# Performance work log

Hardware: AMD Instinct MI355X
Metric: run time of the kernel (lower is better)

The kernel has to match this reference:

```python
import jax, jax.numpy as jnp
import numpy as np

B, S, HID = 4, 2048, 2048
NH, NKV = 8, 1
HD = HID // NH  # 256
G = NH // NKV   # queries per kv head
ROPE_THETA = 10000.0
NEG_INF = -1e9


def setup_inputs() -> dict:
    key = jax.random.key(0)
    ks = jax.random.split(key, 4)
    x = jax.random.normal(ks[0], (B, S, HID), jnp.float32)
    qkv_dim = (NH + 2 * NKV) * HD
    w_qkv = jax.random.normal(ks[1], (HID, qkv_dim), jnp.float32) * (HID ** -0.5)
    b_qkv = jnp.zeros((qkv_dim,), jnp.float32)
    w_o = jax.random.normal(ks[2], (NH * HD, HID), jnp.float32) * ((NH * HD) ** -0.5)
    b_o = jnp.zeros((HID,), jnp.float32)
    # rotary table: cos/sin of position*inv_freq, interleaved-pair convention
    inv_freq = 1.0 / (ROPE_THETA ** (jnp.arange(0, HD, 2, dtype=jnp.float32) / HD))
    ang = jnp.outer(jnp.arange(S, dtype=jnp.float32), inv_freq)  # [S, HD/2]
    freqs_cis = jnp.stack([jnp.cos(ang), jnp.sin(ang)], axis=-1)  # [S, HD/2, 2]
    causal = jnp.tril(jnp.ones((S, S), bool))
    mask = jnp.where(causal, 0.0, NEG_INF).astype(jnp.float32)[None, None]  # [1,1,S,S]
    return dict(x=x, w_qkv=w_qkv, b_qkv=b_qkv, w_o=w_o, b_o=b_o,
                freqs_cis=freqs_cis, mask=mask)


def _rope(t, cos, sin):
    # t: [B,S,H,D]; cos/sin: [1,S,1,D/2]; interleaved complex pairs
    tp = t.reshape(*t.shape[:-1], -1, 2)
    r, i = tp[..., 0], tp[..., 1]
    out = jnp.stack([r * cos - i * sin, r * sin + i * cos], axis=-1)
    return out.reshape(t.shape)


def reference(x, w_qkv, b_qkv, w_o, b_o, freqs_cis, mask):
    b, s, _ = x.shape
    qkv = x @ w_qkv + b_qkv
    q, k, v = jnp.split(qkv, [NH * HD, NH * HD + NKV * HD], axis=-1)
    q = q.reshape(b, s, NH, HD)
    k = k.reshape(b, s, NKV, HD)
    v = v.reshape(b, s, NKV, HD)
    cos = freqs_cis[..., 0][None, :, None, :]
    sin = freqs_cis[..., 1][None, :, None, :]
    q = _rope(q, cos, sin)
    k = _rope(k, cos, sin)
    # GQA: head h attends with kv group h // G (same layout as repeat_interleave)
    qh = q.transpose(0, 2, 1, 3).reshape(b, NKV, G, s, HD)  # [B,KV,G,S,D]
    kh = k.transpose(0, 2, 1, 3)                            # [B,KV,S,D]
    vh = v.transpose(0, 2, 1, 3)
    scores = jnp.einsum('bkgqd,bksd->bkgqs', qh, kh) * (HD ** -0.5)
    scores = scores + mask[:, :, None]  # broadcast over group dim
    attn = jax.nn.softmax(scores.astype(jnp.float32), axis=-1).astype(q.dtype)
    out = jnp.einsum('bkgqs,bksd->bkgqd', attn, vh)         # [B,KV,G,S,D]
    out = out.reshape(b, NH, s, HD).transpose(0, 2, 1, 3).reshape(b, s, NH * HD)
    return out @ w_o + b_o
```

## Files before the change

### kernel.cpp

```cpp
#include <hip/hip_runtime.h>
#include <hip/hip_bf16.h>

#define B_ 4
#define S_ 2048
#define HID_ 2048
#define NH_ 8
#define HD_ 256
#define QKVN 2560

typedef unsigned short u16;
typedef unsigned long long ull;
typedef __attribute__((ext_vector_type(4))) float f32x4;
typedef __attribute__((ext_vector_type(16))) float f32x16;
typedef __attribute__((ext_vector_type(8))) short bf16x8;

__device__ __forceinline__ float bf2f(u16 u) {
  union { unsigned int i; float f; } v; v.i = ((unsigned int)u) << 16; return v.f;
}
__device__ __forceinline__ u16 f2bf(float f) {
  union { unsigned int i; float f; } v; v.f = f;
  unsigned int r = v.i + 0x7fffu + ((v.i >> 16) & 1u);
  return (u16)(r >> 16);
}

__global__ void cast_f32_bf16(const float* __restrict__ in, u16* __restrict__ out, int n8) {
  int i = blockIdx.x * blockDim.x + threadIdx.x;
  int stride = gridDim.x * blockDim.x;
  for (; i < n8; i += stride) {
    const float4* p = (const float4*)(in + (size_t)i * 8);
    float4 a = p[0], b = p[1];
    u16 o[8] = {f2bf(a.x), f2bf(a.y), f2bf(a.z), f2bf(a.w),
                f2bf(b.x), f2bf(b.y), f2bf(b.z), f2bf(b.w)};
    *(uint4*)(out + (size_t)i * 8) = *(const uint4*)o;
  }
}

__global__ void transpose_cast(const float* __restrict__ in, u16* __restrict__ out, int R, int C) {
  __shared__ float t[32][33];
  int c0 = blockIdx.x * 32, r0 = blockIdx.y * 32;
  int tx = threadIdx.x, ty = threadIdx.y;
#pragma unroll
  for (int i = 0; i < 4; ++i)
    t[ty + i * 8][tx] = in[(size_t)(r0 + ty + i * 8) * C + c0 + tx];
  __syncthreads();
#pragma unroll
  for (int i = 0; i < 4; ++i)
    out[(size_t)(c0 + ty + i * 8) * R + r0 + tx] = f2bf(t[tx][ty + i * 8]);
}

__global__ void transpose_bf16(const u16* __restrict__ in, u16* __restrict__ out, int R, int C) {
  __shared__ u16 t[32][33];
  in += (size_t)blockIdx.z * R * C;
  out += (size_t)blockIdx.z * R * C;
  int c0 = blockIdx.x * 32, r0 = blockIdx.y * 32;
  int tx = threadIdx.x, ty = threadIdx.y;
#pragma unroll
  for (int i = 0; i < 4; ++i)
    t[ty + i * 8][tx] = in[(size_t)(r0 + ty + i * 8) * C + c0 + tx];
  __syncthreads();
#pragma unroll
  for (int i = 0; i < 4; ++i)
    out[(size_t)(c0 + ty + i * 8) * R + r0 + tx] = t[tx][ty + i * 8];
}

template <bool OUT_F32>
__global__ __launch_bounds__(256) void gemm_bt(const u16* __restrict__ A, const u16* __restrict__ BT,
                                               const float* __restrict__ bias, void* __restrict__ Cout,
                                               int M, int N, int K) {
  __shared__ u16 As[128 * 32];
  __shared__ u16 Bs[128 * 32];
  int nwg = gridDim.x;
  int bid = (int)blockIdx.x;
  bid = (bid & 7) * (nwg >> 3) + (bid >> 3);
  int ntiles = N >> 7;
  int m0 = (bid / ntiles) << 7, n0 = (bid % ntiles) << 7;
  int tid = threadIdx.x, w = tid >> 6, lane = tid & 63;
  int wr = w >> 1, wc = w & 1;
  int l15 = lane & 15, lg = lane >> 4;
  f32x4 acc[4][4] = {};
  int crow = lane >> 2;
  int ccol = (lane & 3) * 8;
  for (int k0 = 0; k0 < K; k0 += 32) {
#pragma unroll
    for (int i = 0; i < 2; ++i) {
      int c = w * 2 + i;
      const u16* ga = A + (size_t)(m0 + c * 16 + crow) * K + k0 + ccol;
      const u16* gb = BT + (size_t)(n0 + c * 16 + crow) * K + k0 + ccol;
      __builtin_amdgcn_global_load_lds((const __attribute__((address_space(1))) void*)ga,
                                       (__attribute__((address_space(3))) void*)(As + c * 512), 16, 0, 0);
      __builtin_amdgcn_global_load_lds((const __attribute__((address_space(1))) void*)gb,
                                       (__attribute__((address_space(3))) void*)(Bs + c * 512), 16, 0, 0);
    }
    __syncthreads();
    bf16x8 af[4], bfr[4];
#pragma unroll
    for (int r = 0; r < 4; ++r)
      af[r] = *(const bf16x8*)&As[(wr * 64 + r * 16 + l15) * 32 + lg * 8];
#pragma unroll
    for (int c = 0; c < 4; ++c)
      bfr[c] = *(const bf16x8*)&Bs[(wc * 64 + c * 16 + l15) * 32 + lg * 8];
#pragma unroll
    for (int r = 0; r < 4; ++r)
#pragma unroll
      for (int c = 0; c < 4; ++c)
        acc[r][c] = __builtin_amdgcn_mfma_f32_16x16x32_bf16(af[r], bfr[c], acc[r][c], 0, 0, 0);
    __syncthreads();
  }
#pragma unroll
  for (int r = 0; r < 4; ++r) {
    int mrow = m0 + wr * 64 + r * 16 + lg * 4;
#pragma unroll
    for (int c = 0; c < 4; ++c) {
      int col = n0 + wc * 64 + c * 16 + l15;
      float bv = bias[col];
#pragma unroll
      for (int j = 0; j < 4; ++j) {
        float v = acc[r][c][j] + bv;
        if (OUT_F32)
          ((float*)Cout)[(size_t)(mrow + j) * N + col] = v;
        else
          ((u16*)Cout)[(size_t)(mrow + j) * N + col] = f2bf(v);
      }
    }
  }
}

__global__ void rope_scatter(const u16* __restrict__ qkv, const float* __restrict__ freqs,
                             u16* __restrict__ qo, u16* __restrict__ ko, u16* __restrict__ vo) {
  const int per_row = QKVN / 8;
  const int total = B_ * S_ * per_row;
  int i = blockIdx.x * blockDim.x + threadIdx.x;
  int stride = gridDim.x * blockDim.x;
  for (; i < total; i += stride) {
    int m = i / per_row;
    int n8 = (i - m * per_row) * 8;
    int b = m >> 11, s = m & 2047;
    uint4 raw = *(const uint4*)(qkv + (size_t)m * QKVN + n8);
    const u16* u = (const u16*)&raw;
    if (n8 < 2304) {
      int d = (n8 < 2048) ? (n8 & 255) : (n8 - 2048);
      float scl = (n8 < 2048) ? (0.0625f * 1.44269504f) : 1.0f;
      const float* fp = freqs + ((size_t)s * 128 + (d >> 1)) * 2;
      float4 f0 = *(const float4*)fp;
      float4 f1 = *(const float4*)(fp + 4);
      float fc[8] = {f0.x, f0.y, f0.z, f0.w, f1.x, f1.y, f1.z, f1.w};
      u16 o[8];
#pragma unroll
      for (int p = 0; p < 4; ++p) {
        float r = bf2f(u[2 * p]), im = bf2f(u[2 * p + 1]);
        float c = fc[2 * p], sn = fc[2 * p + 1];
        o[2 * p] = f2bf((r * c - im * sn) * scl);
        o[2 * p + 1] = f2bf((r * sn + im * c) * scl);
      }
      u16* dst;
      if (n8 < 2048) {
        dst = qo + (size_t)m * 2048 + n8;
      } else {
        dst = ko + (((size_t)m) << 8) + d;
      }
      *(uint4*)dst = *(const uint4*)o;
    } else {
      int d = n8 - 2304;
      *(uint4*)(vo + (((size_t)m) << 8) + d) = raw;
    }
  }
}


#define STAGE_K(bufofs, kt)                                                                       \
  do {                                                                                            \
    _Pragma("unroll") for (int _p = 0; _p < 4; ++_p) {                                            \
      int _idx = _p * 512 + tid;                                                                  \
      int _row = _idx >> 5, _c = _idx & 31;                                                       \
      const u16* _src = Kp + ((size_t)(b * S_ + (kt) * 64 + _row)) * HD_ +                        \
                        ((_c ^ (_row & 31)) * 8);                                                 \
      __builtin_amdgcn_global_load_lds(                                                           \
          (const __attribute__((address_space(1))) void*)_src,                                    \
          (__attribute__((address_space(3))) void*)(KsBase + (bufofs) + _idx * 8), 16, 0, 0);     \
    }                                                                                             \
  } while (0)

#define STAGE_V(bufofs, kt)                                                                       \
  do {                                                                                            \
    _Pragma("unroll") for (int _p = 0; _p < 4; ++_p) {                                            \
      int _idx = _p * 512 + tid;                                                                  \
      int _r = _idx >> 4, _gp = _idx & 15;                                                        \
      int _g = _gp ^ (_r & 15);                                                                   \
      int _d = _r * 2 + (_g >> 3), _c = _g & 7;                                                   \
      const u16* _src = VTp + ((size_t)(b * 256 + _d)) * S_ + (kt) * 64 + _c * 8;                 \
      __builtin_amdgcn_global_load_lds(                                                           \
          (const __attribute__((address_space(1))) void*)_src,                                    \
          (__attribute__((address_space(3))) void*)(VsBase + (bufofs) + _idx * 8), 16, 0, 0);     \
    }                                                                                             \
  } while (0)

#define FLASH_SEG_BODY()                                                                          \
  STAGE_K(0, kb);                                                                                 \
  STAGE_V(0, kb);                                                                                 \
  __syncthreads();                                                                                \
  int cur = 0;                                                                                    \
  for (int kt = kb; kt < ke; ++kt) {                                                              \
    if (kt + 1 < ke) {                                                                            \
      STAGE_K((cur ^ 1) * 16384, kt + 1);                                                         \
      STAGE_V((cur ^ 1) * 16384, kt + 1);                                                         \
    }                                                                                             \
    const char* Kb = (const char*)(KsBase + cur * 16384);                                         \
    const char* Vb = (const char*)(VsBase + cur * 16384);                                         \
    _Pragma("unroll") for (int tau = 0; tau < 2; ++tau) {                                         \
      int k0 = kt * 64 + tau * 32;                                                                \
      if (k0 > t * 32 + 31) break;                                                                \
      int row = tau * 32 + l31;                                                                   \
      f32x16 scv = {};                                                                            \
      __builtin_amdgcn_s_setprio(1);                                                              \
      _Pragma("unroll") for (int st = 0; st < 16; ++st) {                                         \
        bf16x8 kf = *(const bf16x8*)(Kb + row * 512 + (((st * 2 + lh) ^ l31) << 4));              \
        scv = __builtin_amdgcn_mfma_f32_32x32x16_bf16(kf, qf[st], scv, 0, 0, 0);                  \
      }                                                                                           \
      __builtin_amdgcn_s_setprio(0);                                                              \
      if (k0 + 31 > t * 32) {                                                                     \
        _Pragma("unroll") for (int jj = 0; jj < 16; ++jj) {                                       \
          int kg = k0 + (jj & 3) + 8 * (jj >> 2) + 4 * lh;                                        \
          if (kg > s_g) scv[jj] = -3.0e38f;                                                       \
        }                                                                                         \
      }                                                                                           \
      float tmax = -3.0e38f;                                                                      \
      _Pragma("unroll") for (int jj = 0; jj < 16; ++jj) tmax = fmaxf(tmax, scv[jj]);              \
      tmax = fmaxf(tmax, __shfl_xor(tmax, 32));                                                   \
      if (!__all(tmax - m_r <= 8.0f)) {                                                           \
        float mnew = fmaxf(m_r, tmax);                                                            \
        float sc = exp2f(m_r - mnew);                                                             \
        l_r *= sc;                                                                                \
        _Pragma("unroll") for (int dt = 0; dt < 8; ++dt) oacc[dt] *= sc;                          \
        m_r = mnew;                                                                               \
      }                                                                                           \
      float ts = 0.f;                                                                             \
      unsigned cpk[8];                                                                            \
      _Pragma("unroll") for (int mi = 0; mi < 8; ++mi) {                                          \
        float p0 = exp2f(scv[2 * mi] - m_r);                                                      \
        float p1 = exp2f(scv[2 * mi + 1] - m_r);                                                  \
        ts += p0 + p1;                                                                            \
        cpk[mi] = ((unsigned)f2bf(p1) << 16) | f2bf(p0);                                          \
      }                                                                                           \
      ts += __shfl_xor(ts, 32);                                                                   \
      l_r += ts;                                                                                  \
      asm volatile("v_permlane32_swap_b32 %0, %1" : "+v"(cpk[0]), "+v"(cpk[2]));                  \
      asm volatile("v_permlane32_swap_b32 %0, %1" : "+v"(cpk[1]), "+v"(cpk[3]));                  \
      asm volatile("v_permlane32_swap_b32 %0, %1" : "+v"(cpk[4]), "+v"(cpk[6]));                  \
      asm volatile("v_permlane32_swap_b32 %0, %1" : "+v"(cpk[5]), "+v"(cpk[7]));                  \
      union { unsigned u[4]; bf16x8 v; } pa, pb;                                                  \
      pa.u[0] = cpk[0]; pa.u[1] = cpk[1]; pa.u[2] = cpk[2]; pa.u[3] = cpk[3];                     \
      pb.u[0] = cpk[4]; pb.u[1] = cpk[5]; pb.u[2] = cpk[6]; pb.u[3] = cpk[7];                     \
      __builtin_amdgcn_s_setprio(1);                                                              \
      _Pragma("unroll") for (int dt = 0; dt < 8; ++dt) {                                          \
        int d = dt * 32 + l31;                                                                    \
        int rr = d >> 1;                                                                          \
        int gb = (d & 1) * 8 + tau * 4;                                                           \
        int rx = (rr & 15) << 4;                                                                  \
        bf16x8 va = *(const bf16x8*)(Vb + rr * 256 + (((gb + lh) << 4) ^ rx));                    \
        oacc[dt] = __builtin_amdgcn_mfma_f32_32x32x16_bf16(va, pa.v, oacc[dt], 0, 0, 0);          \
        bf16x8 vb2 = *(const bf16x8*)(Vb + rr * 256 + (((gb + 2 + lh) << 4) ^ rx));               \
        oacc[dt] = __builtin_amdgcn_mfma_f32_32x32x16_bf16(vb2, pb.v, oacc[dt], 0, 0, 0);         \
      }                                                                                           \
      __builtin_amdgcn_s_setprio(0);                                                              \
    }                                                                                             \
    __syncthreads();                                                                              \
    cur ^= 1;                                                                                     \
  }

__global__ __launch_bounds__(512, 2) void flash_attn(const u16* __restrict__ Qp, const u16* __restrict__ Kp,
                                                     const u16* __restrict__ VTp, u16* __restrict__ Op) {
  __shared__ u16 Ks[2][64 * 256];
  __shared__ u16 Vs[2][128 * 128];
  int bid = (int)blockIdx.x;
  int b = bid & 3, t = bid >> 2;
  int tid = threadIdx.x;
  int w = tid >> 6, l = tid & 63;
  int l31 = l & 31, lh = l >> 5;
  int q_local = w * 32 + l31;
  size_t qrow = (size_t)b * 16384 + (size_t)t * 256 + q_local;
  int s_g = t * 32 + (q_local >> 3);
  u16* KsBase = &Ks[0][0];
  u16* VsBase = &Vs[0][0];
  bf16x8 qf[16];
  const u16* qp = Qp + qrow * HD_ + lh * 8;
#pragma unroll
  for (int st = 0; st < 16; ++st) qf[st] = *(const bf16x8*)(qp + st * 16);
  f32x16 oacc[8] = {};
  float m_r = -3.0e38f, l_r = 0.f;
  int kb = 0, ke = t / 2 + 1;
  FLASH_SEG_BODY();
  float inv = 1.0f / l_r;
  u16* ob = Op + qrow * 256;
#pragma unroll
  for (int dt = 0; dt < 8; ++dt) {
#pragma unroll
    for (int jj = 0; jj < 4; ++jj) {
      int d0 = dt * 32 + jj * 8 + 4 * lh;
      u16 o4[4];
#pragma unroll
      for (int e = 0; e < 4; ++e) o4[e] = f2bf(oacc[dt][jj * 4 + e] * inv);
      *(ull*)(ob + d0) = *(const ull*)o4;
    }
  }
}

__global__ __launch_bounds__(512, 2) void flash_attn_split(const u16* __restrict__ Qp, const u16* __restrict__ Kp,
                                                           const u16* __restrict__ VTp, u16* __restrict__ P0,
                                                           float* __restrict__ ml0, float* __restrict__ ml1,
                                                           u16* __restrict__ Op) {
  __shared__ u16 Ks[2][64 * 256];
  __shared__ u16 Vs[2][128 * 128];
  int bid = (int)blockIdx.x;
  int b = (bid & 7) >> 1;
  int j = ((bid & 1) << 5) + (bid >> 3);
  int tid = threadIdx.x;
  int w = tid >> 6, l = tid & 63;
  int l31 = l & 31, lh = l >> 5;
  int q_local = w * 32 + l31;
  u16* KsBase = &Ks[0][0];
  u16* VsBase = &Vs[0][0];

  for (int seg = 0; seg < 2; ++seg) {
    int t = seg ? (63 - j) : j;
    int nkv = (t >> 1) + 1;
    int half = (nkv + 1) >> 1;
    int kb = seg ? half : 0;
    int ke = seg ? nkv : half;
    size_t qrow = (size_t)b * 16384 + (size_t)t * 256 + q_local;
    int s_g = t * 32 + (q_local >> 3);
    float* mlbuf = seg ? ml1 : ml0;
    if (kb >= ke) {
      if (lh == 0) { mlbuf[qrow * 2] = -3.0e38f; mlbuf[qrow * 2 + 1] = 0.f; }
      continue;
    }
    bf16x8 qf[16];
    const u16* qp = Qp + qrow * HD_ + lh * 8;
#pragma unroll
    for (int st = 0; st < 16; ++st) qf[st] = *(const bf16x8*)(qp + st * 16);
    f32x16 oacc[8] = {};
    float m_r = -3.0e38f, l_r = 0.f;
    FLASH_SEG_BODY();
    float inv = 1.0f / l_r;
    u16* ob = (seg ? Op : P0) + qrow * 256;
#pragma unroll
    for (int dt = 0; dt < 8; ++dt) {
#pragma unroll
      for (int jj = 0; jj < 4; ++jj) {
        int d0 = dt * 32 + jj * 8 + 4 * lh;
        u16 o4[4];
#pragma unroll
        for (int e = 0; e < 4; ++e) o4[e] = f2bf(oacc[dt][jj * 4 + e] * inv);
        *(ull*)(ob + d0) = *(const ull*)o4;
      }
    }
    if (lh == 0) { mlbuf[qrow * 2] = m_r; mlbuf[qrow * 2 + 1] = l_r; }
  }
}

__global__ __launch_bounds__(256) void combine_parts(const u16* __restrict__ P0, const float* __restrict__ ml0,
                                                     const float* __restrict__ ml1, u16* __restrict__ O) {
  int idx = blockIdx.x * 256 + threadIdx.x;
  int r = idx >> 5;
  int c = (idx & 31) * 8;
  float m0 = ml0[(size_t)r * 2], l0 = ml0[(size_t)r * 2 + 1];
  float m1 = ml1[(size_t)r * 2], l1 = ml1[(size_t)r * 2 + 1];
  float M = fmaxf(m0, m1);
  float w0 = l0 * exp2f(m0 - M), w1 = l1 * exp2f(m1 - M);
  float inv = 1.0f / (w0 + w1);
  w0 *= inv; w1 *= inv;
  uint4 a = *(const uint4*)(P0 + (size_t)r * 256 + c);
  uint4 bq = *(const uint4*)(O + (size_t)r * 256 + c);
  const u16* ua = (const u16*)&a;
  const u16* ub = (const u16*)&bq;
  u16 o[8];
#pragma unroll
  for (int e = 0; e < 8; ++e) o[e] = f2bf(w0 * bf2f(ua[e]) + w1 * bf2f(ub[e]));
  *(uint4*)(O + (size_t)r * 256 + c) = *(const uint4*)o;
}

extern "C" void kernel_launch(void* const* d_in, const int* in_sizes, int n_in,
                              void* d_out, int out_size, void* d_ws, size_t ws_size,
                              hipStream_t stream) {
  const float* x = (const float*)d_in[0];
  const float* w_qkv = (const float*)d_in[1];
  const float* b_qkv = (const float*)d_in[2];
  const float* w_o = (const float*)d_in[3];
  const float* b_o = (const float*)d_in[4];
  const float* freqs = (const float*)d_in[5];

  char* ws = (char*)d_ws;
  u16* xb    = (u16*)ws;
  u16* wqkvT = (u16*)(ws + 33554432);
  u16* woT   = (u16*)(ws + 44040192);
  u16* qkv   = (u16*)(ws + 52428800);
  u16* qall  = (u16*)(ws + 94371840);
  u16* kbuf  = (u16*)(ws + 127926272);
  u16* vbuf  = (u16*)(ws + 132120576);
  u16* part0 = (u16*)(ws + 136314880);
  float* ml0 = (float*)(ws + 169869312);
  float* ml1 = (float*)(ws + 170393600);
  u16* vT    = xb;
  u16* attout = qkv;

  bool split = (ws_size >= 170917888ULL);

  cast_f32_bf16<<<2048, 256, 0, stream>>>(x, xb, (B_ * S_ * HID_) / 8);
  transpose_cast<<<dim3(QKVN / 32, HID_ / 32), dim3(32, 8), 0, stream>>>(w_qkv, wqkvT, HID_, QKVN);
  transpose_cast<<<dim3(HID_ / 32, HID_ / 32), dim3(32, 8), 0, stream>>>(w_o, woT, HID_, HID_);
  gemm_bt<false><<<dim3(64 * 20), 256, 0, stream>>>(xb, wqkvT, b_qkv, qkv, B_ * S_, QKVN, HID_);
  rope_scatter<<<2048, 256, 0, stream>>>(qkv, freqs, qall, kbuf, vbuf);
  transpose_bf16<<<dim3(HD_ / 32, S_ / 32, B_), dim3(32, 8), 0, stream>>>(vbuf, vT, S_, HD_);
  if (split) {
    flash_attn_split<<<256, 512, 0, stream>>>(qall, kbuf, vT, part0, ml0, ml1, attout);
    combine_parts<<<8192, 256, 0, stream>>>(part0, ml0, ml1, attout);
  } else {
    flash_attn<<<256, 512, 0, stream>>>(qall, kbuf, vT, attout);
  }
  gemm_bt<true><<<dim3(64 * 16), 256, 0, stream>>>(attout, woT, b_o, d_out, B_ * S_, HID_, HID_);
}
```

Before: 421.7 us.

## Replace GEMM with 256x256-tile double-buffered pipelined MFMA kernel

Replaces the simple 128x128, BK=32 single-buffered bf16 GEMM used for the QKV and output projections with a 256x256-tile, BK=64, 512-thread kernel. It double-buffers LDS and interleaves global->LDS staging with MFMA phases, using explicit vmcnt waits, barriers and s_setprio. An XOR swizzle is added to avoid LDS bank conflicts. The goal is to hide memory latency and raise arithmetic intensity per loaded tile. The cost is larger LDS use (128KB per block) and fewer workgroups: 320 and 256 blocks on a device with 256 CUs, which leaves tail imbalance for the QKV GEMM.

```diff
diff --git a/kernel.cpp b/kernel.cpp
--- a/kernel.cpp
+++ b/kernel.cpp
@@ -63,59 +63,130 @@
     out[(size_t)(c0 + ty + i * 8) * R + r0 + tx] = t[tx][ty + i * 8];
 }
 
+#define BAR() __builtin_amdgcn_s_barrier()
+#define PRIO1() __builtin_amdgcn_s_setprio(1)
+#define PRIO0() __builtin_amdgcn_s_setprio(0)
+#define SB0() __builtin_amdgcn_sched_barrier(0)
+#define WVM(n)                                                                                    \
+  do {                                                                                            \
+    SB0();                                                                                        \
+    asm volatile("s_waitcnt vmcnt(" #n ")" ::: "memory");                                         \
+    SB0();                                                                                        \
+  } while (0)
+
+#define STG(mat, b0, h, T, ldsb)                                                                  \
+  do {                                                                                            \
+    _Pragma("unroll") for (int q = 0; q < 2; ++q) {                                               \
+      int idx = q * 512 + tid;                                                                    \
+      int rl = idx >> 3, gp = idx & 7;                                                            \
+      const u16* s = (mat) + (size_t)((b0) + (h) * 128 + rl) * K + (T) * 64 +                     \
+                     ((gp ^ (rl & 7)) << 3);                                                      \
+      __builtin_amdgcn_global_load_lds((const __attribute__((address_space(1))) void*)s,          \
+          (__attribute__((address_space(3))) void*)((ldsb) + (h) * 8192 + idx * 8), 16, 0, 0);    \
+    }                                                                                             \
+  } while (0)
+
+#define LOAD_A(buf, mib)                                                                          \
+  _Pragma("unroll") for (int mi = 0; mi < 4; ++mi)                                                \
+  _Pragma("unroll") for (int ks = 0; ks < 2; ++ks)                                                \
+    af[mi][ks] = *(const bf16x8*)((buf) + (wr * 128 + ((mib) + mi) * 16 + l15) * 64 +             \
+                                  (((ks * 4 + lg) ^ (l15 & 7)) << 3));
+
+#define LOAD_B(buf, nib)                                                                          \
+  _Pragma("unroll") for (int ni = 0; ni < 2; ++ni)                                                \
+  _Pragma("unroll") for (int ks = 0; ks < 2; ++ks)                                                \
+    bfr[(nib) + ni][ks] = *(const bf16x8*)((buf) + (wc * 64 + ((nib) + ni) * 16 + l15) * 64 +     \
+                                           (((ks * 4 + lg) ^ (l15 & 7)) << 3));
+
+#define MFMA16(accb, nib)                                                                         \
+  _Pragma("unroll") for (int mi = 0; mi < 4; ++mi)                                                \
+  _Pragma("unroll") for (int ni = 0; ni < 2; ++ni)                                                \
+  _Pragma("unroll") for (int ks = 0; ks < 2; ++ks)                                                \
+    acc[(accb) + mi][(nib) + ni] = __builtin_amdgcn_mfma_f32_16x16x32_bf16(                       \
+        af[mi][ks], bfr[(nib) + ni][ks], acc[(accb) + mi][(nib) + ni], 0, 0, 0);
+
 template <bool OUT_F32>
-__global__ __launch_bounds__(256) void gemm_bt(const u16* __restrict__ A, const u16* __restrict__ BT,
-                                               const float* __restrict__ bias, void* __restrict__ Cout,
-                                               int M, int N, int K) {
-  __shared__ u16 As[128 * 32];
-  __shared__ u16 Bs[128 * 32];
+__global__ __launch_bounds__(512, 2) void gemm256(const u16* __restrict__ A, const u16* __restrict__ BT,
+                                                  const float* __restrict__ bias, void* __restrict__ Cout,
+                                                  int M, int N, int K) {
+  __shared__ u16 Asm[2][16384];
+  __shared__ u16 Bsm[2][16384];
   int nwg = gridDim.x;
   int bid = (int)blockIdx.x;
   bid = (bid & 7) * (nwg >> 3) + (bid >> 3);
-  int ntiles = N >> 7;
-  int m0 = (bid / ntiles) << 7, n0 = (bid % ntiles) << 7;
+  int ntn = N >> 8;
+  int m0 = (bid / ntn) << 8, n0 = (bid % ntn) << 8;
   int tid = threadIdx.x, w = tid >> 6, lane = tid & 63;
-  int wr = w >> 1, wc = w & 1;
+  int wr = w >> 2, wc = w & 3;
   int l15 = lane & 15, lg = lane >> 4;
-  f32x4 acc[4][4] = {};
-  int crow = lane >> 2;
-  int ccol = (lane & 3) * 8;
-  for (int k0 = 0; k0 < K; k0 += 32) {
-#pragma unroll
-    for (int i = 0; i < 2; ++i) {
-      int c = w * 2 + i;
-      const u16* ga = A + (size_t)(m0 + c * 16 + crow) * K + k0 + ccol;
-      const u16* gb = BT + (size_t)(n0 + c * 16 + crow) * K + k0 + ccol;
-      __builtin_amdgcn_global_load_lds((const __attribute__((address_space(1))) void*)ga,
-                                       (__attribute__((address_space(3))) void*)(As + c * 512), 16, 0, 0);
-      __builtin_amdgcn_global_load_lds((const __attribute__((address_space(1))) void*)gb,
-                                       (__attribute__((address_space(3))) void*)(Bs + c * 512), 16, 0, 0);
-    }
-    __syncthreads();
-    bf16x8 af[4], bfr[4];
-#pragma unroll
-    for (int r = 0; r < 4; ++r)
-      af[r] = *(const bf16x8*)&As[(wr * 64 + r * 16 + l15) * 32 + lg * 8];
-#pragma unroll
-    for (int c = 0; c < 4; ++c)
-      bfr[c] = *(const bf16x8*)&Bs[(wc * 64 + c * 16 + l15) * 32 + lg * 8];
-#pragma unroll
-    for (int r = 0; r < 4; ++r)
-#pragma unroll
-      for (int c = 0; c < 4; ++c)
-        acc[r][c] = __builtin_amdgcn_mfma_f32_16x16x32_bf16(af[r], bfr[c], acc[r][c], 0, 0, 0);
-    __syncthreads();
-  }
-#pragma unroll
-  for (int r = 0; r < 4; ++r) {
-    int mrow = m0 + wr * 64 + r * 16 + lg * 4;
-#pragma unroll
-    for (int c = 0; c < 4; ++c) {
-      int col = n0 + wc * 64 + c * 16 + l15;
+  int NT = K >> 6;
+  u16* A0b = &Asm[0][0]; u16* A1b = &Asm[1][0];
+  u16* B0b = &Bsm[0][0]; u16* B1b = &Bsm[1][0];
+  f32x4 acc[8][4] = {};
+  bf16x8 af[4][2], bfr[4][2];
+
+  STG(A, m0, 0, 0, A0b); STG(A, m0, 1, 0, A0b);
+  STG(BT, n0, 0, 0, B0b); STG(BT, n0, 1, 0, B0b);
+  STG(A, m0, 0, 1, A1b); STG(BT, n0, 0, 1, B1b);
+  WVM(0);
+  BAR();
+
+  for (int T = 0; T + 2 < NT; T += 2) {
+    LOAD_A(A0b, 0); LOAD_B(B0b, 0);
+    STG(A, m0, 1, T + 1, A1b);
+    BAR(); PRIO1(); MFMA16(0, 0); PRIO0(); BAR();
+    LOAD_B(B0b, 2);
+    STG(BT, n0, 1, T + 1, B1b);
+    BAR(); PRIO1(); MFMA16(0, 2); PRIO0(); BAR();
+    LOAD_A(A0b, 4);
+    STG(BT, n0, 0, T + 2, B0b);
+    BAR(); PRIO1(); MFMA16(4, 0); PRIO0(); BAR();
+    STG(A, m0, 0, T + 2, A0b);
+    WVM(4);
+    BAR(); PRIO1(); MFMA16(4, 2); PRIO0(); BAR();
+    LOAD_A(A1b, 0); LOAD_B(B1b, 0);
+    STG(A, m0, 1, T + 2, A0b);
+    BAR(); PRIO1(); MFMA16(0, 0); PRIO0(); BAR();
+    LOAD_B(B1b, 2);
+    STG(BT, n0, 1, T + 2, B0b);
+    BAR(); PRIO1(); MFMA16(0, 2); PRIO0(); BAR();
+    LOAD_A(A1b, 4);
+    STG(BT, n0, 0, T + 3, B1b);
+    BAR(); PRIO1(); MFMA16(4, 0); PRIO0(); BAR();
+    STG(A, m0, 0, T + 3, A1b);
+    WVM(4);
+    BAR(); PRIO1(); MFMA16(4, 2); PRIO0(); BAR();
+  }
+  {
+    int T = NT - 2;
+    LOAD_A(A0b, 0); LOAD_B(B0b, 0);
+    STG(A, m0, 1, T + 1, A1b);
+    BAR(); PRIO1(); MFMA16(0, 0); PRIO0(); BAR();
+    LOAD_B(B0b, 2);
+    STG(BT, n0, 1, T + 1, B1b);
+    BAR(); PRIO1(); MFMA16(0, 2); PRIO0(); BAR();
+    LOAD_A(A0b, 4);
+    BAR(); PRIO1(); MFMA16(4, 0); PRIO0(); BAR();
+    WVM(0);
+    BAR(); PRIO1(); MFMA16(4, 2); PRIO0(); BAR();
+    LOAD_A(A1b, 0); LOAD_B(B1b, 0);
+    BAR(); PRIO1(); MFMA16(0, 0); PRIO0(); BAR();
+    LOAD_B(B1b, 2);
+    BAR(); PRIO1(); MFMA16(0, 2); PRIO0(); BAR();
+    LOAD_A(A1b, 4);
+    BAR(); PRIO1(); MFMA16(4, 0); PRIO0(); BAR();
+    PRIO1(); MFMA16(4, 2); PRIO0();
+  }
+#pragma unroll
+  for (int mi = 0; mi < 8; ++mi) {
+    int mrow = m0 + wr * 128 + mi * 16 + lg * 4;
+#pragma unroll
+    for (int ni = 0; ni < 4; ++ni) {
+      int col = n0 + wc * 64 + ni * 16 + l15;
       float bv = bias[col];
 #pragma unroll
       for (int j = 0; j < 4; ++j) {
-        float v = acc[r][c][j] + bv;
+        float v = acc[mi][ni][j] + bv;
         if (OUT_F32)
           ((float*)Cout)[(size_t)(mrow + j) * N + col] = v;
         else
@@ -165,7 +236,6 @@
     }
   }
 }
-
 
 #define STAGE_K(bufofs, kt)                                                                       \
   do {                                                                                            \
@@ -407,7 +477,7 @@
   cast_f32_bf16<<<2048, 256, 0, stream>>>(x, xb, (B_ * S_ * HID_) / 8);
   transpose_cast<<<dim3(QKVN / 32, HID_ / 32), dim3(32, 8), 0, stream>>>(w_qkv, wqkvT, HID_, QKVN);
   transpose_cast<<<dim3(HID_ / 32, HID_ / 32), dim3(32, 8), 0, stream>>>(w_o, woT, HID_, HID_);
-  gemm_bt<false><<<dim3(64 * 20), 256, 0, stream>>>(xb, wqkvT, b_qkv, qkv, B_ * S_, QKVN, HID_);
+  gemm256<false><<<dim3(32 * 10), 512, 0, stream>>>(xb, wqkvT, b_qkv, qkv, B_ * S_, QKVN, HID_);
   rope_scatter<<<2048, 256, 0, stream>>>(qkv, freqs, qall, kbuf, vbuf);
   transpose_bf16<<<dim3(HD_ / 32, S_ / 32, B_), dim3(32, 8), 0, stream>>>(vbuf, vT, S_, HD_);
   if (split) {
@@ -416,5 +486,5 @@
   } else {
     flash_attn<<<256, 512, 0, stream>>>(qall, kbuf, vT, attout);
   }
-  gemm_bt<true><<<dim3(64 * 16), 256, 0, stream>>>(attout, woT, b_o, d_out, B_ * S_, HID_, HID_);
-}
+  gemm256<true><<<dim3(32 * 8), 512, 0, stream>>>(attout, woT, b_o, d_out, B_ * S_, HID_, HID_);
+}
```

After: 398.0 us. 1.06x faster.
